# Kernel optimization log

Measured on AMD Instinct MI355X. Metric: run time of the kernel, lower is better.

Reference implementation:

```python
import jax, jax.numpy as jnp
import numpy as np

B = 64; PAST = 128; FUTURE = 64; HID = 64; HEADS = 4
F = 16 + 8 + 24 + 3  # out_preprocess = 51


def _pre(cat, num, emb0, emb1, emb2):
    # pre_processing: embedding lookups per categorical column + last 3 float cols
    return jnp.concatenate([emb0[cat[:, 0]], emb1[cat[:, 1]], emb2[cat[:, 2]], num], axis=-1)


def _gat_conv(x, edge_index, lin_w, att_src, att_dst, bias, heads, out_ch):
    # PyG GATConv: concat=False (head mean), add_self_loops=True, leaky_relu slope 0.2
    N = x.shape[0]
    loops = jnp.arange(N, dtype=edge_index.dtype)
    src = jnp.concatenate([edge_index[0], loops])
    dst = jnp.concatenate([edge_index[1], loops])
    h = (x @ lin_w).reshape(N, heads, out_ch)          # [N, H, C]
    a_src = (h * att_src).sum(-1)                      # [N, H]
    a_dst = (h * att_dst).sum(-1)
    e = jax.nn.leaky_relu(a_src[src] + a_dst[dst], 0.2)  # [E, H]
    m = jax.lax.stop_gradient(jax.ops.segment_max(e, dst, num_segments=N))
    ex = jnp.exp(e - m[dst])
    s = jax.ops.segment_sum(ex, dst, num_segments=N)
    alpha = ex / (s[dst] + 1e-16)                      # softmax over in-edges per node
    out = jax.ops.segment_sum(alpha[:, :, None] * h[src], dst, num_segments=N)
    return out.mean(1) + bias                          # concat=False -> mean over heads


def setup_inputs() -> dict:
    ks = jax.random.split(jax.random.key(0), 17)
    N1, N2 = B * PAST, B * FUTURE
    E1, E2 = N1 * 16, N2 * 16
    return dict(
        cat1=jax.random.randint(ks[0], (N1, 3), 0, 7),
        num1=jax.random.normal(ks[1], (N1, 3), dtype=jnp.float32),
        cat2=jax.random.randint(ks[2], (N2, 3), 0, 7),
        num2=jax.random.normal(ks[3], (N2, 3), dtype=jnp.float32),
        e1=jax.random.randint(ks[4], (2, E1), 0, N1),
        e2=jax.random.randint(ks[5], (2, E2), 0, N2),
        A=jax.random.randint(ks[6], (PAST + FUTURE, PAST + FUTURE), 0, 2),
        emb0=0.1 * jax.random.normal(ks[7], (24, 16), dtype=jnp.float32),
        emb1=0.1 * jax.random.normal(ks[8], (7, 8), dtype=jnp.float32),
        emb2=0.1 * jax.random.normal(ks[9], (500, 24), dtype=jnp.float32),
        g1_lin=0.1 * jax.random.normal(ks[10], (F, HEADS * (F - 1)), dtype=jnp.float32),
        g1_asrc=0.1 * jax.random.normal(ks[11], (HEADS, F - 1), dtype=jnp.float32),
        g1_adst=0.1 * jax.random.normal(ks[12], (HEADS, F - 1), dtype=jnp.float32),
        g1_b=jnp.zeros((F - 1,), dtype=jnp.float32),
        g2_lin=0.1 * jax.random.normal(ks[13], (F, HEADS), dtype=jnp.float32),
        g2_asrc=0.1 * jax.random.normal(ks[14], (HEADS, 1), dtype=jnp.float32),
        g2_adst=0.1 * jax.random.normal(ks[15], (HEADS, 1), dtype=jnp.float32),
        g2_b=jnp.zeros((1,), dtype=jnp.float32),
        W=0.1 * jax.random.normal(ks[16], (F - 1, HID), dtype=jnp.float32),
    )


def reference(cat1, num1, cat2, num2, e1, e2, A, emb0, emb1, emb2,
              g1_lin, g1_asrc, g1_adst, g1_b, g2_lin, g2_asrc, g2_adst, g2_b, W):
    x = _pre(cat1, num1, emb0, emb1, emb2)                       # [B*PAST, F]
    x2 = _pre(cat2, num2, emb0, emb1, emb2).reshape(B, FUTURE, F)
    x1 = _gat_conv(x, e1, g1_lin, g1_asrc, g1_adst, g1_b, HEADS, F - 1).reshape(B, PAST, F - 1)
    # pairwise diff between every (future, past) node pair within a graph
    diff = x1[:, None, :, :] - x2[:, :, None, :F - 1]            # [B, FUTURE, PAST, F-1]
    M = W @ W.T
    M = M + M.T                                                  # WW^T + (WW^T)^T
    # original builds full [PAST, PAST] quadratic form and extracts diagonal;
    # compute only the diagonal: -0.5 * diff_i M diff_i
    alpha = -0.5 * jnp.einsum('bfpd,de,bfpe->bfp', diff, M, diff)
    mask = A[:PAST, PAST:].T                                     # [FUTURE, PAST]
    alpha = jnp.where(mask == 0, -jnp.inf, alpha)
    alpha = jax.nn.softmax(alpha, axis=-1)
    y_past = x.reshape(B, PAST, F)[:, :, -1:]                    # [B, PAST, 1]
    tmp = alpha @ y_past                                         # [B, FUTURE, 1]
    x2b = jnp.concatenate([x2[:, :, :F - 1], tmp], axis=-1)
    out = _gat_conv(x2b.reshape(-1, F), e2, g2_lin, g2_asrc, g2_adst, g2_b, HEADS, 1)
    return out.reshape(B, FUTURE)
```

## Files before the change

kernel.cpp:

```cpp
#include <hip/hip_runtime.h>

static constexpr int B_ = 64, PAST = 128, FUTURE = 64, F_ = 51;
static constexpr int N1 = B_ * PAST;
static constexpr int N2 = B_ * FUTURE;
static constexpr int E1 = N1 * 16;
static constexpr int E2 = N2 * 16;
static constexpr int MAXDEG = 64;
static constexpr int XITEMS = E1 + N1 + E2 + N2 + FUTURE * PAST;
static constexpr int PASTB = N1 / 4;
static constexpr int FUTB  = N2 / 4;
static constexpr int XB    = XITEMS / 256;
static constexpr int POISON_I = (int)0xAAAAAAAA;

__device__ __forceinline__ int depoison(int v) {
    int d = v - POISON_I;
    return (d >= 0 && d < 1000000) ? d : v;
}

__device__ __forceinline__
float node_feat(const int* cat, const float* num, const float* e0, const float* e1,
                const float* e2, int n, int t) {
    if (t < 16) return e0[cat[n * 3 + 0] * 16 + t];
    if (t < 24) return e1[cat[n * 3 + 1] * 8 + (t - 16)];
    if (t < 48) return e2[cat[n * 3 + 2] * 24 + (t - 24)];
    return num[n * 3 + (t - 48)];
}

__global__ __launch_bounds__(256) void k_prep(
        const int* __restrict__ cat1, const float* __restrict__ num1,
        const int* __restrict__ cat2, const float* __restrict__ num2,
        const int* __restrict__ e1, const int* __restrict__ e2,
        const int* __restrict__ A,
        const float* __restrict__ emb0, const float* __restrict__ emb1,
        const float* __restrict__ emb2,
        const float* __restrict__ g1_lin, const float* __restrict__ g1_asrc,
        const float* __restrict__ g1_adst, const float* __restrict__ W,
        float* __restrict__ h1, float* __restrict__ asrc1, float* __restrict__ adst1,
        float* __restrict__ y1, float* __restrict__ x2g, float* __restrict__ P2,
        int* __restrict__ count1, int* __restrict__ slot1,
        int* __restrict__ count2, int* __restrict__ slot2,
        int* __restrict__ maskT) {
    int blk = blockIdx.x, t = threadIdx.x;
    int lane = t & 63, wv = t >> 6;

    if (blk < PASTB) {
        int n = blk * 4 + wv;
        float xv = (lane < F_) ? node_feat(cat1, num1, emb0, emb1, emb2, n, lane) : 0.f;
        if (lane == 50) y1[n] = xv;
        float acc0 = 0.f, acc1 = 0.f, acc2 = 0.f, acc3 = 0.f;
        #pragma unroll
        for (int j = 0; j < F_; ++j) {
            float xj = __shfl(xv, j);
            const float* g = g1_lin + j * 200;
            acc0 += xj * g[lane];
            acc1 += xj * g[64 + lane];
            acc2 += xj * g[128 + lane];
            if (lane < 8) acc3 += xj * g[192 + lane];
        }
        float* hr = h1 + n * 200;
        hr[lane] = acc0; hr[64 + lane] = acc1; hr[128 + lane] = acc2;
        if (lane < 8) hr[192 + lane] = acc3;
        float ga0 = g1_asrc[lane], ga1 = g1_asrc[64 + lane], ga2 = g1_asrc[128 + lane];
        float gd0 = g1_adst[lane], gd1 = g1_adst[64 + lane], gd2 = g1_adst[128 + lane];
        float ga3 = (lane < 8) ? g1_asrc[192 + lane] : 0.f;
        float gd3 = (lane < 8) ? g1_adst[192 + lane] : 0.f;
        float s0 = (lane < 50) ? acc0 * ga0 : 0.f;
        float s1 = ((lane >= 50) ? acc0 * ga0 : 0.f) + ((lane < 36) ? acc1 * ga1 : 0.f);
        float s2 = ((lane >= 36) ? acc1 * ga1 : 0.f) + ((lane < 22) ? acc2 * ga2 : 0.f);
        float s3 = ((lane >= 22) ? acc2 * ga2 : 0.f) + ((lane < 8) ? acc3 * ga3 : 0.f);
        float d0 = (lane < 50) ? acc0 * gd0 : 0.f;
        float d1 = ((lane >= 50) ? acc0 * gd0 : 0.f) + ((lane < 36) ? acc1 * gd1 : 0.f);
        float d2 = ((lane >= 36) ? acc1 * gd1 : 0.f) + ((lane < 22) ? acc2 * gd2 : 0.f);
        float d3 = ((lane >= 22) ? acc2 * gd2 : 0.f) + ((lane < 8) ? acc3 * gd3 : 0.f);
        #pragma unroll
        for (int m = 32; m >= 1; m >>= 1) {
            s0 += __shfl_xor(s0, m); s1 += __shfl_xor(s1, m);
            s2 += __shfl_xor(s2, m); s3 += __shfl_xor(s3, m);
            d0 += __shfl_xor(d0, m); d1 += __shfl_xor(d1, m);
            d2 += __shfl_xor(d2, m); d3 += __shfl_xor(d3, m);
        }
        if (lane < 8) {
            int h = lane & 3;
            float vS = (h == 0) ? s0 : (h == 1) ? s1 : (h == 2) ? s2 : s3;
            float vD = (h == 0) ? d0 : (h == 1) ? d1 : (h == 2) ? d2 : d3;
            if (lane < 4) asrc1[n * 4 + h] = vS;
            else          adst1[n * 4 + h] = vD;
        }
        return;
    }

    if (blk < PASTB + FUTB) {
        int n = (blk - PASTB) * 4 + wv;
        float xv = (lane < F_) ? node_feat(cat2, num2, emb0, emb1, emb2, n, lane) : 0.f;
        if (lane < F_) x2g[n * F_ + lane] = xv;
        float acc = 0.f;
        #pragma unroll
        for (int j = 0; j < 50; ++j) acc += __shfl(xv, j) * W[j * 64 + lane];
        P2[n * 64 + lane] = acc;
        return;
    }

    int i = (blk - PASTB - FUTB) * 256 + t;
    if (i < E1) {
        int src = e1[i], dst = e1[E1 + i];
        int pos = depoison(atomicAdd(&count1[dst], 1));
        if (pos < MAXDEG) slot1[dst * MAXDEG + pos] = src;
    } else if (i < E1 + N1) {
        int n = i - E1;
        int pos = depoison(atomicAdd(&count1[n], 1));
        if (pos < MAXDEG) slot1[n * MAXDEG + pos] = n;
    } else if (i < E1 + N1 + E2) {
        int k = i - E1 - N1;
        int src = e2[k], dst = e2[E2 + k];
        int pos = depoison(atomicAdd(&count2[dst], 1));
        if (pos < MAXDEG) slot2[dst * MAXDEG + pos] = src;
    } else if (i < E1 + N1 + E2 + N2) {
        int n = i - E1 - N1 - E2;
        int pos = depoison(atomicAdd(&count2[n], 1));
        if (pos < MAXDEG) slot2[n * MAXDEG + pos] = n;
    } else {
        int k = i - (E1 + N1 + E2 + N2);
        int f = k >> 7, pp = k & 127;
        maskT[k] = A[pp * 192 + PAST + f];
    }
}

__global__ __launch_bounds__(256) void k_gat1(
        const int* __restrict__ count1, const int* __restrict__ slot1,
        const float* __restrict__ h1, const float* __restrict__ asrc1,
        const float* __restrict__ adst1, const float* __restrict__ g1_b,
        const float* __restrict__ W, float* __restrict__ P1) {
    __shared__ int   Ssrc[4][64];
    __shared__ float Sw[4][4][64];
    __shared__ float Sx[4][64];
    int t = threadIdx.x, lane = t & 63, wv = t >> 6;
    int n = (blockIdx.x * 256 + t) >> 6;
    int deg = min(depoison(count1[n]), MAXDEG);
    int my_src = (lane < deg) ? slot1[n * MAXDEG + lane] : 0;
    float ad0 = adst1[n * 4 + 0], ad1 = adst1[n * 4 + 1];
    float ad2 = adst1[n * 4 + 2], ad3 = adst1[n * 4 + 3];
    float ex0 = 0.f, ex1 = 0.f, ex2 = 0.f, ex3 = 0.f;
    if (lane < deg) {
        float e0 = asrc1[my_src * 4 + 0] + ad0;
        float e1 = asrc1[my_src * 4 + 1] + ad1;
        float e2 = asrc1[my_src * 4 + 2] + ad2;
        float e3 = asrc1[my_src * 4 + 3] + ad3;
        e0 = e0 >= 0.f ? e0 : 0.2f * e0;  ex0 = __expf(e0);
        e1 = e1 >= 0.f ? e1 : 0.2f * e1;  ex1 = __expf(e1);
        e2 = e2 >= 0.f ? e2 : 0.2f * e2;  ex2 = __expf(e2);
        e3 = e3 >= 0.f ? e3 : 0.2f * e3;  ex3 = __expf(e3);
    }
    float s0 = ex0, s1 = ex1, s2 = ex2, s3 = ex3;
    #pragma unroll
    for (int m = 32; m >= 1; m >>= 1) {
        s0 += __shfl_xor(s0, m);
        s1 += __shfl_xor(s1, m);
        s2 += __shfl_xor(s2, m);
        s3 += __shfl_xor(s3, m);
    }
    Ssrc[wv][lane] = my_src;
    Sw[wv][0][lane] = ex0 / (s0 + 1e-16f);
    Sw[wv][1][lane] = ex1 / (s1 + 1e-16f);
    Sw[wv][2][lane] = ex2 / (s2 + 1e-16f);
    Sw[wv][3][lane] = ex3 / (s3 + 1e-16f);
    __syncthreads();
    float acc0 = 0.f, acc1 = 0.f, acc2 = 0.f, acc3 = 0.f;
    for (int i = 0; i < deg; ++i) {
        int srci = Ssrc[wv][i];
        float w0 = Sw[wv][0][i], w1 = Sw[wv][1][i];
        float w2 = Sw[wv][2][i], w3 = Sw[wv][3][i];
        if (lane < 50) {
            const float* hr = &h1[srci * 200];
            acc0 += w0 * hr[lane];
            acc1 += w1 * hr[50 + lane];
            acc2 += w2 * hr[100 + lane];
            acc3 += w3 * hr[150 + lane];
        }
    }
    if (lane < 50)
        Sx[wv][lane] = 0.25f * (acc0 + acc1 + acc2 + acc3) + g1_b[lane];
    __syncthreads();
    float a = 0.f;
    #pragma unroll
    for (int j = 0; j < 50; ++j) a += Sx[wv][j] * W[j * 64 + lane];
    P1[n * 64 + lane] = a;
}

__global__ __launch_bounds__(256) void k_attn(
        const float* __restrict__ P1, const float* __restrict__ P2,
        const int* __restrict__ maskT, const float* __restrict__ y1,
        const float* __restrict__ x2g, const float* __restrict__ g2_lin,
        float* __restrict__ h2g) {
    __shared__ float P1s[64 * 129];
    __shared__ float ys[128];
    int b = blockIdx.x >> 3, fg = blockIdx.x & 7;
    int t = threadIdx.x, lane = t & 63, wv = t >> 6;
    const float* P1b = P1 + b * 8192;
    for (int i = t; i < 8192; i += 256) {
        int pp = i >> 6, kk = i & 63;
        P1s[kk * 129 + pp] = P1b[i];
    }
    if (t < 128) ys[t] = y1[b * 128 + t];
    __syncthreads();
    for (int j = 0; j < 2; ++j) {
        int f = fg * 8 + wv * 2 + j;
        int q = b * 64 + f;
        float p2k = P2[q * 64 + lane];
        float d2a = 0.f, d2b = 0.f;
        for (int k = 0; k < 64; ++k) {
            float bk = __shfl(p2k, k);
            float va = P1s[k * 129 + lane] - bk;
            float vb = P1s[k * 129 + 64 + lane] - bk;
            d2a += va * va;
            d2b += vb * vb;
        }
        int ma = maskT[f * 128 + lane];
        int mb = maskT[f * 128 + 64 + lane];
        float va = ma ? -d2a : -1e30f;
        float vb = mb ? -d2b : -1e30f;
        float mx = fmaxf(va, vb);
        #pragma unroll
        for (int m = 32; m >= 1; m >>= 1) mx = fmaxf(mx, __shfl_xor(mx, m));
        float wa = ma ? __expf(va - mx) : 0.f;
        float wb = mb ? __expf(vb - mx) : 0.f;
        float sw = wa + wb;
        float sy = wa * ys[lane] + wb * ys[64 + lane];
        #pragma unroll
        for (int m = 32; m >= 1; m >>= 1) {
            sw += __shfl_xor(sw, m);
            sy += __shfl_xor(sy, m);
        }
        float tsh = sy / sw;
        float xv = (lane < 50) ? x2g[q * F_ + lane] : 0.f;
        #pragma unroll
        for (int h = 0; h < 4; ++h) {
            float c = xv * g2_lin[lane * 4 + h];
            #pragma unroll
            for (int m = 32; m >= 1; m >>= 1) c += __shfl_xor(c, m);
            c += tsh * g2_lin[50 * 4 + h];
            if (lane == h) h2g[q * 4 + h] = c;
        }
    }
}

__global__ __launch_bounds__(256) void k_gat2(
        const int* __restrict__ count2, const int* __restrict__ slot2,
        const float* __restrict__ h2g, const float* __restrict__ g2_asrc,
        const float* __restrict__ g2_adst, const float* __restrict__ g2_b,
        float* __restrict__ out) {
    int wave = (blockIdx.x * blockDim.x + threadIdx.x) >> 6;
    int lane = threadIdx.x & 63;
    if (wave >= N2) return;
    int n = wave;
    int deg = min(depoison(count2[n]), MAXDEG);
    int my_src = (lane < deg) ? slot2[n * MAXDEG + lane] : 0;
    float ex[4], nm[4], adterm[4], as[4];
    #pragma unroll
    for (int h = 0; h < 4; ++h) {
        as[h] = g2_asrc[h];
        adterm[h] = h2g[n * 4 + h] * g2_adst[h];
        ex[h] = 0.f; nm[h] = 0.f;
    }
    if (lane < deg) {
        #pragma unroll
        for (int h = 0; h < 4; ++h) {
            float hs = h2g[my_src * 4 + h];
            float e = hs * as[h] + adterm[h];
            e = e >= 0.f ? e : 0.2f * e;
            float xv = __expf(e);
            ex[h] = xv;
            nm[h] = xv * hs;
        }
    }
    #pragma unroll
    for (int m = 32; m >= 1; m >>= 1) {
        #pragma unroll
        for (int h = 0; h < 4; ++h) {
            ex[h] += __shfl_xor(ex[h], m);
            nm[h] += __shfl_xor(nm[h], m);
        }
    }
    if (lane == 0) {
        float o = 0.f;
        #pragma unroll
        for (int h = 0; h < 4; ++h) o += nm[h] / (ex[h] + 1e-16f);
        out[n] = 0.25f * o + g2_b[0];
    }
}

extern "C" void kernel_launch(void* const* d_in, const int* in_sizes, int n_in,
                              void* d_out, int out_size, void* d_ws, size_t ws_size,
                              hipStream_t stream) {
    const int*   cat1    = (const int*)  d_in[0];
    const float* num1    = (const float*)d_in[1];
    const int*   cat2    = (const int*)  d_in[2];
    const float* num2    = (const float*)d_in[3];
    const int*   e1      = (const int*)  d_in[4];
    const int*   e2      = (const int*)  d_in[5];
    const int*   A       = (const int*)  d_in[6];
    const float* emb0    = (const float*)d_in[7];
    const float* emb1    = (const float*)d_in[8];
    const float* emb2    = (const float*)d_in[9];
    const float* g1_lin  = (const float*)d_in[10];
    const float* g1_asrc = (const float*)d_in[11];
    const float* g1_adst = (const float*)d_in[12];
    const float* g1_b    = (const float*)d_in[13];
    const float* g2_lin  = (const float*)d_in[14];
    const float* g2_asrc = (const float*)d_in[15];
    const float* g2_adst = (const float*)d_in[16];
    const float* g2_b    = (const float*)d_in[17];
    const float* W       = (const float*)d_in[18];
    float* out = (float*)d_out;

    int*   count1 = (int*)d_ws;
    int*   count2 = count1 + N1;
    int*   slot1  = count2 + N2;
    int*   slot2  = slot1 + N1 * MAXDEG;
    int*   maskT  = slot2 + N2 * MAXDEG;
    float* h1     = (float*)(maskT + FUTURE * PAST);
    float* asrc1  = h1 + N1 * 200;
    float* adst1  = asrc1 + N1 * 4;
    float* y1     = adst1 + N1 * 4;
    float* x2g    = y1 + N1;
    float* P1     = x2g + N2 * F_;
    float* P2     = P1 + N1 * 64;
    float* h2g    = P2 + N2 * 64;

    k_prep<<<PASTB + FUTB + XB, 256, 0, stream>>>(cat1, num1, cat2, num2, e1, e2, A,
                                                  emb0, emb1, emb2,
                                                  g1_lin, g1_asrc, g1_adst, W,
                                                  h1, asrc1, adst1, y1, x2g, P2,
                                                  count1, slot1, count2, slot2, maskT);
    k_gat1<<<N1 / 4, 256, 0, stream>>>(count1, slot1, h1, asrc1, adst1, g1_b, W, P1);
    k_attn<<<B_ * 8, 256, 0, stream>>>(P1, P2, maskT, y1, x2g, g2_lin, h2g);
    k_gat2<<<N2 / 4, 256, 0, stream>>>(count2, slot2, h2g, g2_asrc, g2_adst, g2_b, out);
}
```

Before: 181.1 us.

## Fold GAT1 linear and W projection into precomputed weights, aggregate raw features

A new k_pre kernel folds the GAT1 linear weights into the downstream W projection (M = lin_h·W), into the attention vectors (atS/atD = lin_h·att) and into the bias term (bW = b·W). k_prep therefore no longer computes or stores the 200-wide per-node h1. It stores only the 51-wide input features and takes the attention logits as dot products with atS/atD. k_gat1 gathers 51-wide source features instead of 200-wide rows, keeps M in LDS, and processes 4 nodes per wave to amortise loading it. This reduces gather traffic and intermediate storage, at the cost of an extra small launch and per-node LDS matvecs, with a slight change in floating-point association.

```diff
diff --git a/kernel.cpp b/kernel.cpp
--- a/kernel.cpp
+++ b/kernel.cpp
@@ -26,6 +26,41 @@
     return num[n * 3 + (t - 48)];
 }
 
+__global__ __launch_bounds__(256) void k_pre(
+        const float* __restrict__ g1_lin, const float* __restrict__ g1_asrc,
+        const float* __restrict__ g1_adst, const float* __restrict__ g1_b,
+        const float* __restrict__ W,
+        float* __restrict__ M, float* __restrict__ atS, float* __restrict__ atD,
+        float* __restrict__ bW) {
+    int blk = blockIdx.x, t = threadIdx.x;
+    if (blk < 51) {
+        int j = blk, h = t >> 6, k = t & 63;
+        const float* g = g1_lin + j * 200 + h * 50;
+        float acc = 0.f;
+        #pragma unroll
+        for (int c = 0; c < 50; ++c) acc += g[c] * W[c * 64 + k];
+        M[(h * 51 + j) * 64 + k] = acc;
+    } else {
+        if (t < 408) {
+            int half = t / 204;
+            int r = t - half * 204;
+            int h = r / 51, j = r - h * 51;
+            const float* g = g1_lin + j * 200 + h * 50;
+            const float* a = (half == 0 ? g1_asrc : g1_adst) + h * 50;
+            float acc = 0.f;
+            #pragma unroll
+            for (int c = 0; c < 50; ++c) acc += g[c] * a[c];
+            (half == 0 ? atS : atD)[h * 51 + j] = acc;
+        } else if (t < 472) {
+            int k = t - 408;
+            float acc = 0.f;
+            #pragma unroll
+            for (int c = 0; c < 50; ++c) acc += g1_b[c] * W[c * 64 + k];
+            bW[k] = acc;
+        }
+    }
+}
+
 __global__ __launch_bounds__(256) void k_prep(
         const int* __restrict__ cat1, const float* __restrict__ num1,
         const int* __restrict__ cat2, const float* __restrict__ num2,
@@ -33,9 +68,9 @@
         const int* __restrict__ A,
         const float* __restrict__ emb0, const float* __restrict__ emb1,
         const float* __restrict__ emb2,
-        const float* __restrict__ g1_lin, const float* __restrict__ g1_asrc,
-        const float* __restrict__ g1_adst, const float* __restrict__ W,
-        float* __restrict__ h1, float* __restrict__ asrc1, float* __restrict__ adst1,
+        const float* __restrict__ atS, const float* __restrict__ atD,
+        const float* __restrict__ W,
+        float* __restrict__ x1f, float* __restrict__ asrc1, float* __restrict__ adst1,
         float* __restrict__ y1, float* __restrict__ x2g, float* __restrict__ P2,
         int* __restrict__ count1, int* __restrict__ slot1,
         int* __restrict__ count2, int* __restrict__ slot2,
@@ -46,32 +81,16 @@
     if (blk < PASTB) {
         int n = blk * 4 + wv;
         float xv = (lane < F_) ? node_feat(cat1, num1, emb0, emb1, emb2, n, lane) : 0.f;
+        if (lane < F_) x1f[n * 51 + lane] = xv;
         if (lane == 50) y1[n] = xv;
-        float acc0 = 0.f, acc1 = 0.f, acc2 = 0.f, acc3 = 0.f;
-        #pragma unroll
-        for (int j = 0; j < F_; ++j) {
-            float xj = __shfl(xv, j);
-            const float* g = g1_lin + j * 200;
-            acc0 += xj * g[lane];
-            acc1 += xj * g[64 + lane];
-            acc2 += xj * g[128 + lane];
-            if (lane < 8) acc3 += xj * g[192 + lane];
-        }
-        float* hr = h1 + n * 200;
-        hr[lane] = acc0; hr[64 + lane] = acc1; hr[128 + lane] = acc2;
-        if (lane < 8) hr[192 + lane] = acc3;
-        float ga0 = g1_asrc[lane], ga1 = g1_asrc[64 + lane], ga2 = g1_asrc[128 + lane];
-        float gd0 = g1_adst[lane], gd1 = g1_adst[64 + lane], gd2 = g1_adst[128 + lane];
-        float ga3 = (lane < 8) ? g1_asrc[192 + lane] : 0.f;
-        float gd3 = (lane < 8) ? g1_adst[192 + lane] : 0.f;
-        float s0 = (lane < 50) ? acc0 * ga0 : 0.f;
-        float s1 = ((lane >= 50) ? acc0 * ga0 : 0.f) + ((lane < 36) ? acc1 * ga1 : 0.f);
-        float s2 = ((lane >= 36) ? acc1 * ga1 : 0.f) + ((lane < 22) ? acc2 * ga2 : 0.f);
-        float s3 = ((lane >= 22) ? acc2 * ga2 : 0.f) + ((lane < 8) ? acc3 * ga3 : 0.f);
-        float d0 = (lane < 50) ? acc0 * gd0 : 0.f;
-        float d1 = ((lane >= 50) ? acc0 * gd0 : 0.f) + ((lane < 36) ? acc1 * gd1 : 0.f);
-        float d2 = ((lane >= 36) ? acc1 * gd1 : 0.f) + ((lane < 22) ? acc2 * gd2 : 0.f);
-        float d3 = ((lane >= 22) ? acc2 * gd2 : 0.f) + ((lane < 8) ? acc3 * gd3 : 0.f);
+        float s0 = 0.f, s1 = 0.f, s2 = 0.f, s3 = 0.f;
+        float d0 = 0.f, d1 = 0.f, d2 = 0.f, d3 = 0.f;
+        if (lane < F_) {
+            s0 = xv * atS[lane];        d0 = xv * atD[lane];
+            s1 = xv * atS[51 + lane];   d1 = xv * atD[51 + lane];
+            s2 = xv * atS[102 + lane];  d2 = xv * atD[102 + lane];
+            s3 = xv * atS[153 + lane];  d3 = xv * atD[153 + lane];
+        }
         #pragma unroll
         for (int m = 32; m >= 1; m >>= 1) {
             s0 += __shfl_xor(s0, m); s1 += __shfl_xor(s1, m);
@@ -79,12 +98,11 @@
             d0 += __shfl_xor(d0, m); d1 += __shfl_xor(d1, m);
             d2 += __shfl_xor(d2, m); d3 += __shfl_xor(d3, m);
         }
-        if (lane < 8) {
-            int h = lane & 3;
-            float vS = (h == 0) ? s0 : (h == 1) ? s1 : (h == 2) ? s2 : s3;
-            float vD = (h == 0) ? d0 : (h == 1) ? d1 : (h == 2) ? d2 : d3;
-            if (lane < 4) asrc1[n * 4 + h] = vS;
-            else          adst1[n * 4 + h] = vD;
+        if (lane == 0) {
+            asrc1[n * 4 + 0] = s0; asrc1[n * 4 + 1] = s1;
+            asrc1[n * 4 + 2] = s2; asrc1[n * 4 + 3] = s3;
+            adst1[n * 4 + 0] = d0; adst1[n * 4 + 1] = d1;
+            adst1[n * 4 + 2] = d2; adst1[n * 4 + 3] = d3;
         }
         return;
     }
@@ -127,63 +145,76 @@
 
 __global__ __launch_bounds__(256) void k_gat1(
         const int* __restrict__ count1, const int* __restrict__ slot1,
-        const float* __restrict__ h1, const float* __restrict__ asrc1,
-        const float* __restrict__ adst1, const float* __restrict__ g1_b,
-        const float* __restrict__ W, float* __restrict__ P1) {
-    __shared__ int   Ssrc[4][64];
-    __shared__ float Sw[4][4][64];
-    __shared__ float Sx[4][64];
+        const float* __restrict__ x1f, const float* __restrict__ asrc1,
+        const float* __restrict__ adst1,
+        const float* __restrict__ M, const float* __restrict__ bW,
+        float* __restrict__ P1) {
+    __shared__ float4 Ms[4 * 13 * 64];
     int t = threadIdx.x, lane = t & 63, wv = t >> 6;
-    int n = (blockIdx.x * 256 + t) >> 6;
-    int deg = min(depoison(count1[n]), MAXDEG);
-    int my_src = (lane < deg) ? slot1[n * MAXDEG + lane] : 0;
-    float ad0 = adst1[n * 4 + 0], ad1 = adst1[n * 4 + 1];
-    float ad2 = adst1[n * 4 + 2], ad3 = adst1[n * 4 + 3];
-    float ex0 = 0.f, ex1 = 0.f, ex2 = 0.f, ex3 = 0.f;
-    if (lane < deg) {
-        float e0 = asrc1[my_src * 4 + 0] + ad0;
-        float e1 = asrc1[my_src * 4 + 1] + ad1;
-        float e2 = asrc1[my_src * 4 + 2] + ad2;
-        float e3 = asrc1[my_src * 4 + 3] + ad3;
-        e0 = e0 >= 0.f ? e0 : 0.2f * e0;  ex0 = __expf(e0);
-        e1 = e1 >= 0.f ? e1 : 0.2f * e1;  ex1 = __expf(e1);
-        e2 = e2 >= 0.f ? e2 : 0.2f * e2;  ex2 = __expf(e2);
-        e3 = e3 >= 0.f ? e3 : 0.2f * e3;  ex3 = __expf(e3);
-    }
-    float s0 = ex0, s1 = ex1, s2 = ex2, s3 = ex3;
-    #pragma unroll
-    for (int m = 32; m >= 1; m >>= 1) {
-        s0 += __shfl_xor(s0, m);
-        s1 += __shfl_xor(s1, m);
-        s2 += __shfl_xor(s2, m);
-        s3 += __shfl_xor(s3, m);
-    }
-    Ssrc[wv][lane] = my_src;
-    Sw[wv][0][lane] = ex0 / (s0 + 1e-16f);
-    Sw[wv][1][lane] = ex1 / (s1 + 1e-16f);
-    Sw[wv][2][lane] = ex2 / (s2 + 1e-16f);
-    Sw[wv][3][lane] = ex3 / (s3 + 1e-16f);
+    float* Msf = (float*)Ms;
+    for (int i = t; i < 4 * 51 * 64; i += 256) {
+        int h = i / (51 * 64);
+        int r = i - h * 51 * 64;
+        int j = r >> 6, k = r & 63;
+        Msf[((h * 13 + (j >> 2)) * 64 + k) * 4 + (j & 3)] = M[i];
+    }
+    {
+        int h = t >> 6, k = t & 63;
+        Msf[((h * 13 + 12) * 64 + k) * 4 + 3] = 0.f;
+    }
+    float bWk = bW[lane];
     __syncthreads();
-    float acc0 = 0.f, acc1 = 0.f, acc2 = 0.f, acc3 = 0.f;
-    for (int i = 0; i < deg; ++i) {
-        int srci = Ssrc[wv][i];
-        float w0 = Sw[wv][0][i], w1 = Sw[wv][1][i];
-        float w2 = Sw[wv][2][i], w3 = Sw[wv][3][i];
-        if (lane < 50) {
-            const float* hr = &h1[srci * 200];
-            acc0 += w0 * hr[lane];
-            acc1 += w1 * hr[50 + lane];
-            acc2 += w2 * hr[100 + lane];
-            acc3 += w3 * hr[150 + lane];
-        }
-    }
-    if (lane < 50)
-        Sx[wv][lane] = 0.25f * (acc0 + acc1 + acc2 + acc3) + g1_b[lane];
-    __syncthreads();
-    float a = 0.f;
-    #pragma unroll
-    for (int j = 0; j < 50; ++j) a += Sx[wv][j] * W[j * 64 + lane];
-    P1[n * 64 + lane] = a;
+
+    for (int rep = 0; rep < 4; ++rep) {
+        int n = blockIdx.x * 16 + wv * 4 + rep;
+        int deg = min(depoison(count1[n]), MAXDEG);
+        int my_src = (lane < deg) ? slot1[n * MAXDEG + lane] : 0;
+        float ad0 = adst1[n * 4 + 0], ad1 = adst1[n * 4 + 1];
+        float ad2 = adst1[n * 4 + 2], ad3 = adst1[n * 4 + 3];
+        float ex0 = 0.f, ex1 = 0.f, ex2 = 0.f, ex3 = 0.f;
+        if (lane < deg) {
+            float e0 = asrc1[my_src * 4 + 0] + ad0;
+            float e1 = asrc1[my_src * 4 + 1] + ad1;
+            float e2 = asrc1[my_src * 4 + 2] + ad2;
+            float e3 = asrc1[my_src * 4 + 3] + ad3;
+            e0 = e0 >= 0.f ? e0 : 0.2f * e0;  ex0 = __expf(e0);
+            e1 = e1 >= 0.f ? e1 : 0.2f * e1;  ex1 = __expf(e1);
+            e2 = e2 >= 0.f ? e2 : 0.2f * e2;  ex2 = __expf(e2);
+            e3 = e3 >= 0.f ? e3 : 0.2f * e3;  ex3 = __expf(e3);
+        }
+        float s0 = ex0, s1 = ex1, s2 = ex2, s3 = ex3;
+        #pragma unroll
+        for (int m = 32; m >= 1; m >>= 1) {
+            s0 += __shfl_xor(s0, m);
+            s1 += __shfl_xor(s1, m);
+            s2 += __shfl_xor(s2, m);
+            s3 += __shfl_xor(s3, m);
+        }
+        float w0 = ex0 / (s0 + 1e-16f), w1 = ex1 / (s1 + 1e-16f);
+        float w2 = ex2 / (s2 + 1e-16f), w3 = ex3 / (s3 + 1e-16f);
+        float xa0 = 0.f, xa1 = 0.f, xa2 = 0.f, xa3 = 0.f;
+        for (int i = 0; i < deg; ++i) {
+            int srci = __shfl(my_src, i);
+            float a0 = __shfl(w0, i), a1 = __shfl(w1, i);
+            float a2 = __shfl(w2, i), a3 = __shfl(w3, i);
+            float xs = (lane < F_) ? x1f[srci * 51 + lane] : 0.f;
+            xa0 += a0 * xs; xa1 += a1 * xs; xa2 += a2 * xs; xa3 += a3 * xs;
+        }
+        float sum = 0.f;
+        #pragma unroll
+        for (int h = 0; h < 4; ++h) {
+            float xah = (h == 0) ? xa0 : (h == 1) ? xa1 : (h == 2) ? xa2 : xa3;
+            #pragma unroll
+            for (int g = 0; g < 13; ++g) {
+                float4 mv = Ms[(h * 13 + g) * 64 + lane];
+                sum += __shfl(xah, 4 * g + 0) * mv.x
+                     + __shfl(xah, 4 * g + 1) * mv.y
+                     + __shfl(xah, 4 * g + 2) * mv.z
+                     + __shfl(xah, 4 * g + 3) * mv.w;
+            }
+        }
+        P1[n * 64 + lane] = bWk + 0.25f * sum;
+    }
 }
 
 __global__ __launch_bounds__(256) void k_attn(
@@ -317,21 +348,25 @@
     int*   slot1  = count2 + N2;
     int*   slot2  = slot1 + N1 * MAXDEG;
     int*   maskT  = slot2 + N2 * MAXDEG;
-    float* h1     = (float*)(maskT + FUTURE * PAST);
-    float* asrc1  = h1 + N1 * 200;
+    float* x1f    = (float*)(maskT + FUTURE * PAST);
+    float* asrc1  = x1f + N1 * 51;
     float* adst1  = asrc1 + N1 * 4;
     float* y1     = adst1 + N1 * 4;
     float* x2g    = y1 + N1;
     float* P1     = x2g + N2 * F_;
     float* P2     = P1 + N1 * 64;
     float* h2g    = P2 + N2 * 64;
-
+    float* M      = h2g + N2 * 4;
+    float* atS    = M + 4 * 51 * 64;
+    float* atD    = atS + 256;
+    float* bW     = atD + 256;
+
+    k_pre<<<52, 256, 0, stream>>>(g1_lin, g1_asrc, g1_adst, g1_b, W, M, atS, atD, bW);
     k_prep<<<PASTB + FUTB + XB, 256, 0, stream>>>(cat1, num1, cat2, num2, e1, e2, A,
-                                                  emb0, emb1, emb2,
-                                                  g1_lin, g1_asrc, g1_adst, W,
-                                                  h1, asrc1, adst1, y1, x2g, P2,
+                                                  emb0, emb1, emb2, atS, atD, W,
+                                                  x1f, asrc1, adst1, y1, x2g, P2,
                                                   count1, slot1, count2, slot2, maskT);
-    k_gat1<<<N1 / 4, 256, 0, stream>>>(count1, slot1, h1, asrc1, adst1, g1_b, W, P1);
+    k_gat1<<<512, 256, 0, stream>>>(count1, slot1, x1f, asrc1, adst1, M, bW, P1);
     k_attn<<<B_ * 8, 256, 0, stream>>>(P1, P2, maskT, y1, x2g, g2_lin, h2g);
     k_gat2<<<N2 / 4, 256, 0, stream>>>(count2, slot2, h2g, g2_asrc, g2_adst, g2_b, out);
 }
```

New measurement: 216.9 us. 1.2x slower.
